# Performance work log

Measured on AMD Instinct MI355X. Metric: run time of the kernel, lower is better.

## Reference

```python
import jax, jax.numpy as jnp
import numpy as np

ID, IH, IW = 8, 16, 16
HEADS, DIM_HEAD = 8, 32
N = ID * IH * IW  # 2048
INNER = HEADS * DIM_HEAD  # 256
TABLE = (2 * ID - 1) * (2 * IH - 1) * (2 * IW - 1)  # 14415


def _relative_index():
    # Faithful replication of the torch buffer computation (including its
    # unconventional offsets: dim2 never offset, dim1 never scaled).
    g = np.meshgrid(np.arange(ID), np.arange(IH), np.arange(IW), indexing='ij')
    coords = np.stack(g).reshape(3, -1)  # (3, N)
    rc = coords[:, :, None] - coords[:, None, :]  # (3, N, N)
    rc = rc.copy()
    rc[0] += (IH - 1) + (ID - 1)
    rc[1] += (IW - 1) + (ID - 1)
    rc[0] *= 2 * IH - 1
    rel = rc.transpose(1, 2, 0).sum(-1).reshape(-1)  # (N*N,)
    return jnp.asarray(rel, dtype=jnp.int32)


def setup_inputs() -> dict:
    key = jax.random.key(0)
    k1, k2, k3, k4, k5 = jax.random.split(key, 5)
    B, C = 4, 256
    x = jax.random.normal(k1, (B, N, C), dtype=jnp.float32)
    w_qkv = jax.random.normal(k2, (C, 3 * INNER), dtype=jnp.float32) * (C ** -0.5)
    bias_table = jax.random.normal(k3, (TABLE, HEADS), dtype=jnp.float32) * 0.02
    w_out = jax.random.normal(k4, (INNER, C), dtype=jnp.float32) * (INNER ** -0.5)
    b_out = jax.random.normal(k5, (C,), dtype=jnp.float32) * 0.02
    return {"x": x, "w_qkv": w_qkv, "bias_table": bias_table,
            "w_out": w_out, "b_out": b_out, "rel_index": _relative_index()}


def reference(x, w_qkv, bias_table, w_out, b_out, rel_index):
    B, n, C = x.shape
    scale = DIM_HEAD ** -0.5
    qkv = x @ w_qkv  # (B, N, 3*h*d)
    qkv = qkv.reshape(B, n, 3, HEADS, DIM_HEAD)
    q = qkv[:, :, 0].transpose(0, 2, 1, 3)  # (B, h, N, d)
    k = qkv[:, :, 1].transpose(0, 2, 1, 3)
    v = qkv[:, :, 2].transpose(0, 2, 1, 3)
    attn = jnp.einsum('bhnd,bhmd->bhnm', q * scale, k)  # (B, h, N, N)
    bias = bias_table[rel_index].reshape(n, n, HEADS).transpose(2, 0, 1)  # (h, N, N)
    attn = jax.nn.softmax(attn + bias[None], axis=-1)
    out = jnp.einsum('bhnm,bhmd->bhnd', attn, v)  # (B, h, N, d)
    out = out.transpose(0, 2, 1, 3).reshape(B, n, INNER)
    return out @ w_out + b_out
```

## Files before the change

kernel.cpp:

```cpp
#include <hip/hip_runtime.h>
#include <hip/hip_bf16.h>
#include <hip/hip_fp16.h>

#define NTOK 2048
#define HEADS 8
#define DHEAD 32
#define CDIM 256
#define BATCH 4

typedef _Float16 f16x8 __attribute__((ext_vector_type(8)));
typedef _Float16 f16x4 __attribute__((ext_vector_type(4)));
typedef float f32x4 __attribute__((ext_vector_type(4)));
typedef __fp16 fp16v2 __attribute__((ext_vector_type(2)));

static __device__ inline f16x4 pack4(float a, float b, float c, float d) {
    fp16v2 lo = __builtin_amdgcn_cvt_pkrtz(a, b);
    fp16v2 hi = __builtin_amdgcn_cvt_pkrtz(c, d);
    union { struct { fp16v2 lo, hi; } p; f16x4 v; } u;
    u.p.lo = lo; u.p.hi = hi;
    return u.v;
}

static __device__ inline f16x8 pack8f(float a, float b, float c, float d,
                                      float e, float f, float g2, float h2) {
    union { struct { fp16v2 a, b, c, d; } p; f16x8 v; } u;
    u.p.a = __builtin_amdgcn_cvt_pkrtz(a, b);
    u.p.b = __builtin_amdgcn_cvt_pkrtz(c, d);
    u.p.c = __builtin_amdgcn_cvt_pkrtz(e, f);
    u.p.d = __builtin_amdgcn_cvt_pkrtz(g2, h2);
    return u.v;
}

static __device__ inline f16x8 pack8(float4 a, float4 b) {
    return pack8f(a.x, a.y, a.z, a.w, b.x, b.y, b.z, b.w);
}

__global__ __launch_bounds__(256) void prep(const float* __restrict__ x,
                                            const float* __restrict__ w_qkv,
                                            const float* __restrict__ w_out,
                                            _Float16* __restrict__ xh,
                                            _Float16* __restrict__ wqkvT,
                                            _Float16* __restrict__ woutT) {
    __shared__ float tl[32][33];
    const int bid = blockIdx.x;
    if (bid < 1024) {
        const int id = bid * 256 + threadIdx.x;
        const int row = id >> 5;
        const int c = id & 31;
        const int kt = c >> 2;
        const int g = c & 3;
        const float4 a = *(const float4*)(x + row * 256 + kt * 32 + g * 8);
        const float4 b = *(const float4*)(x + row * 256 + kt * 32 + g * 8 + 4);
        const int dst = (row >> 4) * 4096 + kt * 512 + (g * 16 + (row & 15)) * 8;
        *(f16x8*)(xh + dst) = pack8(a, b);
    } else if (bid < 1216) {
        const int t = bid - 1024;
        const int kt = t / 24, nt = t - kt * 24;
        const int tx = threadIdx.x & 31, ty = threadIdx.x >> 5;
#pragma unroll
        for (int i = 0; i < 4; ++i) {
            const int r = ty + i * 8;
            tl[r][tx] = w_qkv[(kt * 32 + r) * 768 + nt * 32 + tx];
        }
        __syncthreads();
        if (threadIdx.x < 128) {
            const int nl = threadIdx.x & 31;
            const int g2 = threadIdx.x >> 5;
            const int ntile = (nt * 32 + nl) >> 4;
            const int lane = (nl & 15) + 16 * g2;
            const float* col = &tl[g2 * 8][nl];
            *(f16x8*)(wqkvT + (ntile * 8 + kt) * 512 + lane * 8) =
                pack8f(col[0], col[33], col[66], col[99],
                       col[132], col[165], col[198], col[231]);
        }
    } else {
        const int t = bid - 1216;
        const int kt = t >> 3, nt = t & 7;
        const int tx = threadIdx.x & 31, ty = threadIdx.x >> 5;
#pragma unroll
        for (int i = 0; i < 4; ++i) {
            const int r = ty + i * 8;
            tl[r][tx] = w_out[(kt * 32 + r) * 256 + nt * 32 + tx];
        }
        __syncthreads();
        if (threadIdx.x < 128) {
            const int nl = threadIdx.x & 31;
            const int g2 = threadIdx.x >> 5;
            const int ntile = (nt * 32 + nl) >> 4;
            const int lane = (nl & 15) + 16 * g2;
            const float* col = &tl[g2 * 8][nl];
            *(f16x8*)(woutT + (ntile * 8 + kt) * 512 + lane * 8) =
                pack8f(col[0], col[33], col[66], col[99],
                       col[132], col[165], col[198], col[231]);
        }
    }
}

__global__ __launch_bounds__(256) void qkv_gemm(const _Float16* __restrict__ xh,
                                                const _Float16* __restrict__ wT,
                                                _Float16* __restrict__ qb,
                                                _Float16* __restrict__ kb,
                                                _Float16* __restrict__ vT) {
    __shared__ _Float16 vt_s[64 * 72];
    const int wave = threadIdx.x >> 6;
    const int lane = threadIdx.x & 63;
    const int idx16 = lane & 15;
    const int g = lane >> 4;

    const int m_base = blockIdx.x * 64;
    const int n0 = blockIdx.y * 64 + wave * 16;

    f32x4 acc[4] = {{0.f, 0.f, 0.f, 0.f}, {0.f, 0.f, 0.f, 0.f},
                    {0.f, 0.f, 0.f, 0.f}, {0.f, 0.f, 0.f, 0.f}};

    const _Float16* bp = wT + (size_t)(blockIdx.y * 4 + wave) * 4096 + lane * 8;
    const _Float16* ap = xh + (size_t)(blockIdx.x * 4) * 4096 + lane * 8;

    for (int kt = 0; kt < 8; ++kt) {
        const f16x8 bf = *(const f16x8*)(bp + kt * 512);
#pragma unroll
        for (int m = 0; m < 4; ++m) {
            const f16x8 af = *(const f16x8*)(ap + m * 4096 + kt * 512);
            acc[m] = __builtin_amdgcn_mfma_f32_16x16x32_f16(af, bf, acc[m], 0, 0, 0);
        }
    }

    const int b = m_base >> 11;
    const int nb = m_base & 2047;
    if (blockIdx.y < 8) {
        const int c = n0 + idx16;
        const int which = c >> 8;
        const int h = (c >> 5) & 7;
        const int d = c & 31;
#pragma unroll
        for (int m = 0; m < 4; ++m) {
#pragma unroll
            for (int r = 0; r < 4; ++r) {
                const int n = nb + m * 16 + g * 4 + r;
                const float val = acc[m][r];
                if (which == 0) {
                    qb[((b * HEADS + h) * NTOK + n) * DHEAD + d] =
                        (_Float16)(val * 0.2550565444545147f);
                } else {
                    kb[((b * HEADS + h) * NTOK + n) * DHEAD + d] = (_Float16)val;
                }
            }
        }
    } else {
        const int cp = wave * 16 + idx16;
#pragma unroll
        for (int m = 0; m < 4; ++m) {
            const int kl = m * 16 + g * 4;
            const int dst = (kl & 32) + (((kl >> 2) & 3) << 3) +
                            (((kl >> 4) & 1) << 2);
            *(f16x4*)(vt_s + cp * 72 + dst) =
                pack4(acc[m][0], acc[m][1], acc[m][2], acc[m][3]);
        }
        __syncthreads();
        const int cpo = threadIdx.x >> 2;
        const int part = threadIdx.x & 3;
        const int vidx = (blockIdx.y - 8) * 64 + cpo;
        const int hh = vidx >> 5;
        const int d = vidx & 31;
        const _Float16* src = vt_s + cpo * 72 + part * 16;
        _Float16* dst = vT + ((size_t)(b * HEADS + hh) * DHEAD + d) * NTOK +
                        nb + part * 16;
        *(f16x8*)(dst) = *(const f16x8*)(src);
        *(f16x8*)(dst + 8) = *(const f16x8*)(src + 8);
    }
}

__global__ __launch_bounds__(256, 4) void attn_partial(
    const _Float16* __restrict__ qp, const _Float16* __restrict__ kp,
    const _Float16* __restrict__ vT, const float* __restrict__ bias_table,
    _Float16* __restrict__ pacc, float* __restrict__ pl) {
    __shared__ float ft[4096];
    __shared__ f16x8 sbuf_v[1024];
    char* sbuf = (char*)sbuf_v;

    const int bh = blockIdx.x;
    const int h = bh & 7;
    for (int u = threadIdx.x; u < 1024; u += 256) {
        const float v =
            bias_table[(1023 - u) * HEADS + h] * 1.4426950408889634f - 8.0f;
        ft[4 * u] = v;
        if (u >= 1) ft[4 * u - 3] = v;
        if (u >= 2) ft[4 * u - 6] = v;
        if (u >= 3) ft[4 * u - 9] = v;
    }

    const int wave = threadIdx.x >> 6;
    const int lane = threadIdx.x & 63;
    const int qi = lane & 15;
    const int g = lane >> 4;
    const int q0 = blockIdx.y * 256 + wave * 64;
    const int ks = blockIdx.z;
    const int kstart = ks * 1024;

    const int tid = threadIdx.x;
    const bool isK = tid < 128;
    const int st_row = (tid & 127) >> 2;
    const int st_c16 = tid & 3;
    const int st_dst = (isK ? 0 : 2048) + st_row * 64 +
                       ((st_c16 ^ ((st_row >> 1) & 3)) << 4);
    const _Float16* st_src = isK
        ? kp + ((size_t)bh * NTOK + kstart + st_row) * DHEAD + st_c16 * 8
        : vT + ((size_t)bh * DHEAD + st_row) * NTOK + kstart + st_c16 * 8;
    const int st_stride = isK ? 32 * DHEAD : 32;

    const int swz = (qi >> 1) & 3;
    const int kf0_off = qi * 64 + ((g ^ swz) << 4);
    const int kf1_off = kf0_off + 1024;
    const int va_lo_off = 2048 + qi * 64 + ((g ^ swz) << 4);
    const int va_hi_off = va_lo_off + 1024;

    const int ig0 = q0 + qi;
    const int ib0 = 31 * (ig0 >> 8) + ((ig0 >> 4) & 15) + (ig0 & 15) + 704;
    const int ub0 = 1023 - ib0 + 4 * g;

    f16x8 qf[4];
#pragma unroll
    for (int m = 0; m < 4; ++m)
        qf[m] = *(const f16x8*)(qp + (bh * NTOK + q0 + m * 16 + qi) * DHEAD + g * 8);

    f32x4 acc0[4] = {{0.f, 0.f, 0.f, 0.f}, {0.f, 0.f, 0.f, 0.f},
                     {0.f, 0.f, 0.f, 0.f}, {0.f, 0.f, 0.f, 0.f}};
    f32x4 acc1[4] = {{0.f, 0.f, 0.f, 0.f}, {0.f, 0.f, 0.f, 0.f},
                     {0.f, 0.f, 0.f, 0.f}, {0.f, 0.f, 0.f, 0.f}};
    f32x4 accl[4] = {{0.f, 0.f, 0.f, 0.f}, {0.f, 0.f, 0.f, 0.f},
                     {0.f, 0.f, 0.f, 0.f}, {0.f, 0.f, 0.f, 0.f}};
    const f16x8 ones8 = {(_Float16)1.f, (_Float16)1.f, (_Float16)1.f,
                         (_Float16)1.f, (_Float16)1.f, (_Float16)1.f,
                         (_Float16)1.f, (_Float16)1.f};

    f16x8 stg0 = *(const f16x8*)(st_src);
    f16x8 stg1 = *(const f16x8*)(st_src + st_stride);
    *(f16x8*)(sbuf + st_dst) = stg0;
    *(f16x8*)(sbuf + 4096 + st_dst) = stg1;
    __syncthreads();

    int cur = 0;
    for (int kt2 = 0; kt2 < 16; ++kt2) {
        if (kt2 < 15) {
            stg0 = *(const f16x8*)(st_src + (2 * kt2 + 2) * st_stride);
            stg1 = *(const f16x8*)(st_src + (2 * kt2 + 3) * st_stride);
        }

#pragma unroll
        for (int tp = 0; tp < 2; ++tp) {
            const int kbase = kstart + (kt2 * 2 + tp) * 32;
            const char* bs = sbuf + cur * 8192 + tp * 4096;
            const f16x8 kf0 = *(const f16x8*)(bs + kf0_off);
            const f16x8 kf1 = *(const f16x8*)(bs + kf1_off);
            const f16x8 va_lo = *(const f16x8*)(bs + va_lo_off);
            const f16x8 va_hi = *(const f16x8*)(bs + va_hi_off);

            const int koff = 31 * (kbase >> 8) + ((kbase >> 4) & 15);
            const int u0 = ub0 + koff;

            __builtin_amdgcn_s_setprio(1);
#pragma unroll
            for (int m = 0; m < 4; ++m) {
                const f32x4 c0 = *(const f32x4*)&ft[(u0 - m) << 2];
                const f32x4 c1 = *(const f32x4*)&ft[(u0 - m + 1) << 2];
                f32x4 s0 = __builtin_amdgcn_mfma_f32_16x16x32_f16(kf0, qf[m], c0, 0, 0, 0);
                f32x4 s1 = __builtin_amdgcn_mfma_f32_16x16x32_f16(kf1, qf[m], c1, 0, 0, 0);

                const float p0 = __builtin_amdgcn_exp2f(s0[0]);
                const float p1 = __builtin_amdgcn_exp2f(s0[1]);
                const float p2 = __builtin_amdgcn_exp2f(s0[2]);
                const float p3 = __builtin_amdgcn_exp2f(s0[3]);
                const float p4 = __builtin_amdgcn_exp2f(s1[0]);
                const float p5 = __builtin_amdgcn_exp2f(s1[1]);
                const float p6 = __builtin_amdgcn_exp2f(s1[2]);
                const float p7 = __builtin_amdgcn_exp2f(s1[3]);

                const f16x8 pf = pack8f(p0, p1, p2, p3, p4, p5, p6, p7);

                acc0[m] = __builtin_amdgcn_mfma_f32_16x16x32_f16(va_lo, pf, acc0[m], 0, 0, 0);
                acc1[m] = __builtin_amdgcn_mfma_f32_16x16x32_f16(va_hi, pf, acc1[m], 0, 0, 0);
                accl[m] = __builtin_amdgcn_mfma_f32_16x16x32_f16(ones8, pf, accl[m], 0, 0, 0);
            }
            __builtin_amdgcn_s_setprio(0);
        }

        if (kt2 < 15) {
            *(f16x8*)(sbuf + (cur ^ 1) * 8192 + st_dst) = stg0;
            *(f16x8*)(sbuf + (cur ^ 1) * 8192 + 4096 + st_dst) = stg1;
        }
        __syncthreads();
        cur ^= 1;
    }

    const int part = bh * 2 + ks;
#pragma unroll
    for (int m = 0; m < 4; ++m) {
        const int ig = q0 + m * 16 + qi;
        _Float16* pb = pacc + ((size_t)part * NTOK + ig) * DHEAD;
        *(f16x4*)(pb + g * 4) = pack4(acc0[m][0], acc0[m][1], acc0[m][2], acc0[m][3]);
        *(f16x4*)(pb + 16 + g * 4) = pack4(acc1[m][0], acc1[m][1], acc1[m][2], acc1[m][3]);
        if (g == 0) pl[part * NTOK + ig] = accl[m][0];
    }
}

__global__ __launch_bounds__(256) void out_gemm(const _Float16* __restrict__ pacc,
                                                const float* __restrict__ pl,
                                                const _Float16* __restrict__ woutT,
                                                const float* __restrict__ b_out,
                                                float* __restrict__ out) {
    __shared__ char a_s[64 * 512];
    const int m_base = blockIdx.x * 64;

    for (int it = 0; it < 8; ++it) {
        const int chunk = it * 256 + threadIdx.x;
        const int row = chunk >> 5;
        const int c8 = (chunk & 31) * 8;
        const int q = m_base + row;
        const int b = q >> 11;
        const int n = q & 2047;
        const int hh = c8 >> 5;
        const int part0 = (b * 8 + hh) * 2;
        const int doff = c8 & 31;
        const float l = pl[(part0 + 0) * NTOK + n] + pl[(part0 + 1) * NTOK + n];
        const float inv = 1.f / l;
        float s[8] = {0.f, 0.f, 0.f, 0.f, 0.f, 0.f, 0.f, 0.f};
#pragma unroll
        for (int p = 0; p < 2; ++p) {
            const f16x8 v = *(const f16x8*)(pacc +
                ((size_t)(part0 + p) * NTOK + n) * DHEAD + doff);
#pragma unroll
            for (int e = 0; e < 8; ++e) s[e] += (float)v[e];
        }
        float4 ca = {s[0] * inv, s[1] * inv, s[2] * inv, s[3] * inv};
        float4 cb = {s[4] * inv, s[5] * inv, s[6] * inv, s[7] * inv};
        const int baddr = (row * 512 + c8 * 2) ^ ((row & 7) << 4);
        *(f16x8*)(a_s + baddr) = pack8(ca, cb);
    }
    __syncthreads();

    const int wave = threadIdx.x >> 6;
    const int lane = threadIdx.x & 63;
    const int idx16 = lane & 15;
    const int g = lane >> 4;
    const int n0 = blockIdx.y * 64 + wave * 16;

    f32x4 acc[4] = {{0.f, 0.f, 0.f, 0.f}, {0.f, 0.f, 0.f, 0.f},
                    {0.f, 0.f, 0.f, 0.f}, {0.f, 0.f, 0.f, 0.f}};

    const _Float16* bp = woutT + (size_t)(blockIdx.y * 4 + wave) * 4096 + lane * 8;
    for (int kt = 0; kt < 8; ++kt) {
        const int k0 = kt * 32 + g * 8;
        const f16x8 bf = *(const f16x8*)(bp + kt * 512);
#pragma unroll
        for (int m = 0; m < 4; ++m) {
            const int row = m * 16 + idx16;
            const int baddr = (row * 512 + k0 * 2) ^ ((row & 7) << 4);
            const f16x8 af = *(const f16x8*)(a_s + baddr);
            acc[m] = __builtin_amdgcn_mfma_f32_16x16x32_f16(af, bf, acc[m], 0, 0, 0);
        }
    }

    const int c = n0 + idx16;
    const float bias = b_out[c];
#pragma unroll
    for (int m = 0; m < 4; ++m) {
#pragma unroll
        for (int r = 0; r < 4; ++r) {
            const int tok = m_base + m * 16 + g * 4 + r;
            out[tok * 256 + c] = acc[m][r] + bias;
        }
    }
}

extern "C" void kernel_launch(void* const* d_in, const int* in_sizes, int n_in,
                              void* d_out, int out_size, void* d_ws, size_t ws_size,
                              hipStream_t stream) {
    const float* x = (const float*)d_in[0];
    const float* w_qkv = (const float*)d_in[1];
    const float* bias_table = (const float*)d_in[2];
    const float* w_out = (const float*)d_in[3];
    const float* b_out = (const float*)d_in[4];
    float* out = (float*)d_out;

    _Float16* pacc = (_Float16*)d_ws;
    float* pl = (float*)(pacc + 4194304);
    _Float16* qb = (_Float16*)(pl + 131072);
    _Float16* kb = qb + 2097152;
    _Float16* vT = kb + 2097152;
    _Float16* wqkvT = vT + 2097152;
    _Float16* woutT = wqkvT + 196608;
    _Float16* xh = (_Float16*)pacc;

    prep<<<1280, 256, 0, stream>>>(x, w_qkv, w_out, xh, wqkvT, woutT);
    qkv_gemm<<<dim3(128, 12), 256, 0, stream>>>(xh, wqkvT, qb, kb, vT);
    attn_partial<<<dim3(32, 8, 2), 256, 0, stream>>>(qb, kb, vT, bias_table,
                                                     pacc, pl);
    out_gemm<<<dim3(128, 4), 256, 0, stream>>>(pacc, pl, woutT, b_out, out);
}
```

Measured before the change: 57.45 us.

## Restructure attention K/V staging into a three-register rotating prefetch pipeline

```diff
diff --git a/kernel.cpp b/kernel.cpp
--- a/kernel.cpp
+++ b/kernel.cpp
@@ -170,12 +170,12 @@
     }
 }
 
-__global__ __launch_bounds__(256, 4) void attn_partial(
+__global__ __launch_bounds__(256, 2) void attn_partial(
     const _Float16* __restrict__ qp, const _Float16* __restrict__ kp,
     const _Float16* __restrict__ vT, const float* __restrict__ bias_table,
     _Float16* __restrict__ pacc, float* __restrict__ pl) {
     __shared__ float ft[4096];
-    __shared__ f16x8 sbuf_v[1024];
+    __shared__ f16x8 sbuf_v[512];
     char* sbuf = (char*)sbuf_v;
 
     const int bh = blockIdx.x;
@@ -233,64 +233,68 @@
                          (_Float16)1.f, (_Float16)1.f, (_Float16)1.f,
                          (_Float16)1.f, (_Float16)1.f};
 
-    f16x8 stg0 = *(const f16x8*)(st_src);
-    f16x8 stg1 = *(const f16x8*)(st_src + st_stride);
-    *(f16x8*)(sbuf + st_dst) = stg0;
-    *(f16x8*)(sbuf + 4096 + st_dst) = stg1;
-    __syncthreads();
-
-    int cur = 0;
-    for (int kt2 = 0; kt2 < 16; ++kt2) {
-        if (kt2 < 15) {
-            stg0 = *(const f16x8*)(st_src + (2 * kt2 + 2) * st_stride);
-            stg1 = *(const f16x8*)(st_src + (2 * kt2 + 3) * st_stride);
-        }
-
-#pragma unroll
-        for (int tp = 0; tp < 2; ++tp) {
-            const int kbase = kstart + (kt2 * 2 + tp) * 32;
-            const char* bs = sbuf + cur * 8192 + tp * 4096;
-            const f16x8 kf0 = *(const f16x8*)(bs + kf0_off);
-            const f16x8 kf1 = *(const f16x8*)(bs + kf1_off);
-            const f16x8 va_lo = *(const f16x8*)(bs + va_lo_off);
-            const f16x8 va_hi = *(const f16x8*)(bs + va_hi_off);
-
-            const int koff = 31 * (kbase >> 8) + ((kbase >> 4) & 15);
-            const int u0 = ub0 + koff;
-
-            __builtin_amdgcn_s_setprio(1);
-#pragma unroll
-            for (int m = 0; m < 4; ++m) {
-                const f32x4 c0 = *(const f32x4*)&ft[(u0 - m) << 2];
-                const f32x4 c1 = *(const f32x4*)&ft[(u0 - m + 1) << 2];
-                f32x4 s0 = __builtin_amdgcn_mfma_f32_16x16x32_f16(kf0, qf[m], c0, 0, 0, 0);
-                f32x4 s1 = __builtin_amdgcn_mfma_f32_16x16x32_f16(kf1, qf[m], c1, 0, 0, 0);
-
-                const float p0 = __builtin_amdgcn_exp2f(s0[0]);
-                const float p1 = __builtin_amdgcn_exp2f(s0[1]);
-                const float p2 = __builtin_amdgcn_exp2f(s0[2]);
-                const float p3 = __builtin_amdgcn_exp2f(s0[3]);
-                const float p4 = __builtin_amdgcn_exp2f(s1[0]);
-                const float p5 = __builtin_amdgcn_exp2f(s1[1]);
-                const float p6 = __builtin_amdgcn_exp2f(s1[2]);
-                const float p7 = __builtin_amdgcn_exp2f(s1[3]);
-
-                const f16x8 pf = pack8f(p0, p1, p2, p3, p4, p5, p6, p7);
-
-                acc0[m] = __builtin_amdgcn_mfma_f32_16x16x32_f16(va_lo, pf, acc0[m], 0, 0, 0);
-                acc1[m] = __builtin_amdgcn_mfma_f32_16x16x32_f16(va_hi, pf, acc1[m], 0, 0, 0);
-                accl[m] = __builtin_amdgcn_mfma_f32_16x16x32_f16(ones8, pf, accl[m], 0, 0, 0);
-            }
-            __builtin_amdgcn_s_setprio(0);
-        }
-
-        if (kt2 < 15) {
-            *(f16x8*)(sbuf + (cur ^ 1) * 8192 + st_dst) = stg0;
-            *(f16x8*)(sbuf + (cur ^ 1) * 8192 + 4096 + st_dst) = stg1;
-        }
-        __syncthreads();
-        cur ^= 1;
-    }
+    f16x8 stgA = *(const f16x8*)(st_src);
+    f16x8 stgB = *(const f16x8*)(st_src + st_stride);
+    f16x8 stgC = *(const f16x8*)(st_src + 2 * st_stride);
+    *(f16x8*)(sbuf + st_dst) = stgA;
+    asm volatile("s_waitcnt lgkmcnt(0)" ::: "memory");
+    __builtin_amdgcn_s_barrier();
+
+    auto compute_tile = [&](int i) {
+        const int kbase = kstart + i * 32;
+        const char* bs = sbuf + (i & 1) * 4096;
+        const f16x8 kf0 = *(const f16x8*)(bs + kf0_off);
+        const f16x8 kf1 = *(const f16x8*)(bs + kf1_off);
+        const f16x8 va_lo = *(const f16x8*)(bs + va_lo_off);
+        const f16x8 va_hi = *(const f16x8*)(bs + va_hi_off);
+        const int koff = 31 * (kbase >> 8) + ((kbase >> 4) & 15);
+        const int u0 = ub0 + koff;
+        __builtin_amdgcn_s_setprio(1);
+#pragma unroll
+        for (int m = 0; m < 4; ++m) {
+            const f32x4 c0 = *(const f32x4*)&ft[(u0 - m) << 2];
+            const f32x4 c1 = *(const f32x4*)&ft[(u0 - m + 1) << 2];
+            f32x4 s0 = __builtin_amdgcn_mfma_f32_16x16x32_f16(kf0, qf[m], c0, 0, 0, 0);
+            f32x4 s1 = __builtin_amdgcn_mfma_f32_16x16x32_f16(kf1, qf[m], c1, 0, 0, 0);
+
+            const float p0 = __builtin_amdgcn_exp2f(s0[0]);
+            const float p1 = __builtin_amdgcn_exp2f(s0[1]);
+            const float p2 = __builtin_amdgcn_exp2f(s0[2]);
+            const float p3 = __builtin_amdgcn_exp2f(s0[3]);
+            const float p4 = __builtin_amdgcn_exp2f(s1[0]);
+            const float p5 = __builtin_amdgcn_exp2f(s1[1]);
+            const float p6 = __builtin_amdgcn_exp2f(s1[2]);
+            const float p7 = __builtin_amdgcn_exp2f(s1[3]);
+
+            const f16x8 pf = pack8f(p0, p1, p2, p3, p4, p5, p6, p7);
+
+            acc0[m] = __builtin_amdgcn_mfma_f32_16x16x32_f16(va_lo, pf, acc0[m], 0, 0, 0);
+            acc1[m] = __builtin_amdgcn_mfma_f32_16x16x32_f16(va_hi, pf, acc1[m], 0, 0, 0);
+            accl[m] = __builtin_amdgcn_mfma_f32_16x16x32_f16(ones8, pf, accl[m], 0, 0, 0);
+        }
+        __builtin_amdgcn_s_setprio(0);
+    };
+
+#define PIPE_STEP(I, LSLOT, WSLOT, DOLOAD)                                   \
+    do {                                                                      \
+        if (DOLOAD) LSLOT = *(const f16x8*)(st_src + ((I) + 3) * st_stride);  \
+        *(f16x8*)(sbuf + ((((I) + 1) & 1) * 4096) + st_dst) = WSLOT;          \
+        compute_tile(I);                                                      \
+        asm volatile("s_waitcnt lgkmcnt(0)" ::: "memory");                    \
+        __builtin_amdgcn_s_barrier();                                         \
+    } while (0)
+
+    for (int ii = 0; ii < 30; ii += 3) {
+        PIPE_STEP(ii + 0, stgA, stgB, (ii + 0) <= 28);
+        PIPE_STEP(ii + 1, stgB, stgC, (ii + 1) <= 28);
+        PIPE_STEP(ii + 2, stgC, stgA, (ii + 2) <= 28);
+    }
+    *(f16x8*)(sbuf + ((31 & 1) * 4096) + st_dst) = stgB;
+    compute_tile(30);
+    asm volatile("s_waitcnt lgkmcnt(0)" ::: "memory");
+    __builtin_amdgcn_s_barrier();
+    compute_tile(31);
+#undef PIPE_STEP
 
     const int part = bh * 2 + ks;
 #pragma unroll
```

Measured after the change: 58.40 us. No clear change (+1.7%).

## Drop split-K attention; normalize in-kernel and emit MFMA-fragment layout for out GEMM

Applied to the files above, without the earlier changes.

```diff
diff --git a/kernel.cpp b/kernel.cpp
--- a/kernel.cpp
+++ b/kernel.cpp
@@ -170,10 +170,10 @@
     }
 }
 
-__global__ __launch_bounds__(256, 4) void attn_partial(
+__global__ __launch_bounds__(256, 2) void attn_full(
     const _Float16* __restrict__ qp, const _Float16* __restrict__ kp,
     const _Float16* __restrict__ vT, const float* __restrict__ bias_table,
-    _Float16* __restrict__ pacc, float* __restrict__ pl) {
+    _Float16* __restrict__ aout) {
     __shared__ float ft[4096];
     __shared__ f16x8 sbuf_v[1024];
     char* sbuf = (char*)sbuf_v;
@@ -194,8 +194,6 @@
     const int qi = lane & 15;
     const int g = lane >> 4;
     const int q0 = blockIdx.y * 256 + wave * 64;
-    const int ks = blockIdx.z;
-    const int kstart = ks * 1024;
 
     const int tid = threadIdx.x;
     const bool isK = tid < 128;
@@ -204,8 +202,8 @@
     const int st_dst = (isK ? 0 : 2048) + st_row * 64 +
                        ((st_c16 ^ ((st_row >> 1) & 3)) << 4);
     const _Float16* st_src = isK
-        ? kp + ((size_t)bh * NTOK + kstart + st_row) * DHEAD + st_c16 * 8
-        : vT + ((size_t)bh * DHEAD + st_row) * NTOK + kstart + st_c16 * 8;
+        ? kp + ((size_t)bh * NTOK + st_row) * DHEAD + st_c16 * 8
+        : vT + ((size_t)bh * DHEAD + st_row) * NTOK + st_c16 * 8;
     const int st_stride = isK ? 32 * DHEAD : 32;
 
     const int swz = (qi >> 1) & 3;
@@ -240,15 +238,15 @@
     __syncthreads();
 
     int cur = 0;
-    for (int kt2 = 0; kt2 < 16; ++kt2) {
-        if (kt2 < 15) {
+    for (int kt2 = 0; kt2 < 32; ++kt2) {
+        if (kt2 < 31) {
             stg0 = *(const f16x8*)(st_src + (2 * kt2 + 2) * st_stride);
             stg1 = *(const f16x8*)(st_src + (2 * kt2 + 3) * st_stride);
         }
 
 #pragma unroll
         for (int tp = 0; tp < 2; ++tp) {
-            const int kbase = kstart + (kt2 * 2 + tp) * 32;
+            const int kbase = (kt2 * 2 + tp) * 32;
             const char* bs = sbuf + cur * 8192 + tp * 4096;
             const f16x8 kf0 = *(const f16x8*)(bs + kf0_off);
             const f16x8 kf1 = *(const f16x8*)(bs + kf1_off);
@@ -284,7 +282,7 @@
             __builtin_amdgcn_s_setprio(0);
         }
 
-        if (kt2 < 15) {
+        if (kt2 < 31) {
             *(f16x8*)(sbuf + (cur ^ 1) * 8192 + st_dst) = stg0;
             *(f16x8*)(sbuf + (cur ^ 1) * 8192 + 4096 + st_dst) = stg1;
         }
@@ -292,70 +290,56 @@
         cur ^= 1;
     }
 
-    const int part = bh * 2 + ks;
+    char* ts = sbuf + wave * 4096;
 #pragma unroll
     for (int m = 0; m < 4; ++m) {
-        const int ig = q0 + m * 16 + qi;
-        _Float16* pb = pacc + ((size_t)part * NTOK + ig) * DHEAD;
-        *(f16x4*)(pb + g * 4) = pack4(acc0[m][0], acc0[m][1], acc0[m][2], acc0[m][3]);
-        *(f16x4*)(pb + 16 + g * 4) = pack4(acc1[m][0], acc1[m][1], acc1[m][2], acc1[m][3]);
-        if (g == 0) pl[part * NTOK + ig] = accl[m][0];
-    }
-}
-
-__global__ __launch_bounds__(256) void out_gemm(const _Float16* __restrict__ pacc,
-                                                const float* __restrict__ pl,
+        const float inv = 1.f / accl[m][0];
+        const int row = m * 16 + qi;
+        const int sw = row & 7;
+        *(f16x4*)(ts + row * 64 + ((g ^ sw) << 3)) =
+            pack4(acc0[m][0] * inv, acc0[m][1] * inv,
+                  acc0[m][2] * inv, acc0[m][3] * inv);
+        *(f16x4*)(ts + row * 64 + (((g + 4) ^ sw) << 3)) =
+            pack4(acc1[m][0] * inv, acc1[m][1] * inv,
+                  acc1[m][2] * inv, acc1[m][3] * inv);
+    }
+    __syncthreads();
+    const int b = bh >> 3;
+    const size_t abase = ((size_t)((b * NTOK + q0) >> 4) * 8 + h) * 512;
+#pragma unroll
+    for (int m = 0; m < 4; ++m) {
+        const int row = m * 16 + qi;
+        const int sw = row & 7;
+        const f16x4 lo = *(const f16x4*)(ts + row * 64 + (((2 * g) ^ sw) << 3));
+        const f16x4 hi = *(const f16x4*)(ts + row * 64 + (((2 * g + 1) ^ sw) << 3));
+        union { struct { f16x4 lo, hi; } p; f16x8 v; } u;
+        u.p.lo = lo; u.p.hi = hi;
+        *(f16x8*)(aout + abase + m * 4096 + lane * 8) = u.v;
+    }
+}
+
+__global__ __launch_bounds__(256) void out_gemm(const _Float16* __restrict__ aoutF,
                                                 const _Float16* __restrict__ woutT,
                                                 const float* __restrict__ b_out,
                                                 float* __restrict__ out) {
-    __shared__ char a_s[64 * 512];
-    const int m_base = blockIdx.x * 64;
-
-    for (int it = 0; it < 8; ++it) {
-        const int chunk = it * 256 + threadIdx.x;
-        const int row = chunk >> 5;
-        const int c8 = (chunk & 31) * 8;
-        const int q = m_base + row;
-        const int b = q >> 11;
-        const int n = q & 2047;
-        const int hh = c8 >> 5;
-        const int part0 = (b * 8 + hh) * 2;
-        const int doff = c8 & 31;
-        const float l = pl[(part0 + 0) * NTOK + n] + pl[(part0 + 1) * NTOK + n];
-        const float inv = 1.f / l;
-        float s[8] = {0.f, 0.f, 0.f, 0.f, 0.f, 0.f, 0.f, 0.f};
-#pragma unroll
-        for (int p = 0; p < 2; ++p) {
-            const f16x8 v = *(const f16x8*)(pacc +
-                ((size_t)(part0 + p) * NTOK + n) * DHEAD + doff);
-#pragma unroll
-            for (int e = 0; e < 8; ++e) s[e] += (float)v[e];
-        }
-        float4 ca = {s[0] * inv, s[1] * inv, s[2] * inv, s[3] * inv};
-        float4 cb = {s[4] * inv, s[5] * inv, s[6] * inv, s[7] * inv};
-        const int baddr = (row * 512 + c8 * 2) ^ ((row & 7) << 4);
-        *(f16x8*)(a_s + baddr) = pack8(ca, cb);
-    }
-    __syncthreads();
-
     const int wave = threadIdx.x >> 6;
     const int lane = threadIdx.x & 63;
     const int idx16 = lane & 15;
     const int g = lane >> 4;
+    const int m_base = blockIdx.x * 64;
     const int n0 = blockIdx.y * 64 + wave * 16;
 
     f32x4 acc[4] = {{0.f, 0.f, 0.f, 0.f}, {0.f, 0.f, 0.f, 0.f},
                     {0.f, 0.f, 0.f, 0.f}, {0.f, 0.f, 0.f, 0.f}};
 
     const _Float16* bp = woutT + (size_t)(blockIdx.y * 4 + wave) * 4096 + lane * 8;
+    const _Float16* ap = aoutF + (size_t)(blockIdx.x * 4) * 4096 + lane * 8;
+
     for (int kt = 0; kt < 8; ++kt) {
-        const int k0 = kt * 32 + g * 8;
         const f16x8 bf = *(const f16x8*)(bp + kt * 512);
 #pragma unroll
         for (int m = 0; m < 4; ++m) {
-            const int row = m * 16 + idx16;
-            const int baddr = (row * 512 + k0 * 2) ^ ((row & 7) << 4);
-            const f16x8 af = *(const f16x8*)(a_s + baddr);
+            const f16x8 af = *(const f16x8*)(ap + m * 4096 + kt * 512);
             acc[m] = __builtin_amdgcn_mfma_f32_16x16x32_f16(af, bf, acc[m], 0, 0, 0);
         }
     }
@@ -382,18 +366,16 @@
     const float* b_out = (const float*)d_in[4];
     float* out = (float*)d_out;
 
-    _Float16* pacc = (_Float16*)d_ws;
-    float* pl = (float*)(pacc + 4194304);
-    _Float16* qb = (_Float16*)(pl + 131072);
+    _Float16* aout = (_Float16*)d_ws;
+    _Float16* qb = aout + 2097152;
     _Float16* kb = qb + 2097152;
     _Float16* vT = kb + 2097152;
     _Float16* wqkvT = vT + 2097152;
     _Float16* woutT = wqkvT + 196608;
-    _Float16* xh = (_Float16*)pacc;
+    _Float16* xh = aout;
 
     prep<<<1280, 256, 0, stream>>>(x, w_qkv, w_out, xh, wqkvT, woutT);
     qkv_gemm<<<dim3(128, 12), 256, 0, stream>>>(xh, wqkvT, qb, kb, vT);
-    attn_partial<<<dim3(32, 8, 2), 256, 0, stream>>>(qb, kb, vT, bias_table,
-                                                     pacc, pl);
-    out_gemm<<<dim3(128, 4), 256, 0, stream>>>(pacc, pl, woutT, b_out, out);
-}
+    attn_full<<<dim3(32, 8), 256, 0, stream>>>(qb, kb, vT, bias_table, aout);
+    out_gemm<<<dim3(128, 4), 256, 0, stream>>>(aout, woutT, b_out, out);
+}
```

Result: slower. 65.13 us (+13.4%).
